# Optimization experiments

Measured on AMD Instinct MI355X. Metric: run time of the kernel, lower is better.

The kernel has to match this reference:

```python
import jax, jax.numpy as jnp
import numpy as np

K_NBR = 128        # PyG radius(max_num_neighbors=128)
NEG_FILL = -1e9    # mask value for max-aggregation over invalid neighbors


def fps(pos, m):
    # Farthest point sampling on pos [N,2] -> [m] int32 indices (start at 0).
    n = pos.shape[0]
    def step(carry, _):
        min_d2, last = carry
        d2 = jnp.sum((pos - pos[last]) ** 2, axis=-1)
        min_d2 = jnp.minimum(min_d2, d2)
        nxt = jnp.argmax(min_d2).astype(jnp.int32)
        return (min_d2, nxt), nxt
    init = (jnp.full((n,), 1e10, pos.dtype), jnp.int32(0))
    _, idxs = jax.lax.scan(step, init, None, length=m - 1)
    return jnp.concatenate([jnp.zeros((1,), jnp.int32), idxs])


def set_abstraction(x, pos, ratio, r, W, b):
    # x [B,N,C], pos [B,N,2]. FPS centers, radius neighbors (<=K), PointNetConv
    # message = Linear(cat[x_j, pos_j - pos_i]) (PyG MLP with one layer and
    # plain_last=True is a bare Linear), then max-aggregate per center.
    B, N, C = x.shape
    m = int(N * ratio)
    idx = jax.vmap(lambda p: fps(p, m))(pos)                         # [B,m]
    ctr = jnp.take_along_axis(pos, idx[..., None], axis=1)           # [B,m,2]
    d2 = jnp.sum((ctr[:, :, None, :] - pos[:, None, :, :]) ** 2, -1)  # [B,m,N]
    k = min(K_NBR, N)
    neg_d2, nbr = jax.lax.top_k(-d2, k)                              # [B,m,k]
    valid = (-neg_d2) <= r * r                                       # in-radius mask
    gather = jax.vmap(lambda a, i: a[i])                             # per-sample fancy index
    x_j = gather(x, nbr)                                             # [B,m,k,C]
    rel = gather(pos, nbr) - ctr[:, :, None, :]                      # [B,m,k,2]
    msg = jnp.concatenate([x_j, rel], axis=-1) @ W + b               # [B,m,k,F]
    msg = jnp.where(valid[..., None], msg, NEG_FILL)
    return jnp.max(msg, axis=2), ctr                                 # [B,m,F], [B,m,2]


def encoder(x, zones_ids, lf_W1, lf_b1, lf_W2, lf_b2, c1_W, c1_b, c2_W, c2_b, c3_W, c3_b):
    lf = jnp.tanh(jnp.tanh(x @ lf_W1 + lf_b1) @ lf_W2 + lf_b2)       # [B,N,64]
    h = jnp.concatenate([lf, zones_ids], axis=-1)                    # [B,N,65]
    h, pos = set_abstraction(h, x, 0.5, 0.5, c1_W, c1_b)             # [B,N/2,64]
    h, pos = set_abstraction(h, pos, 0.25, 1.0, c2_W, c2_b)          # [B,N/8,128]
    g = jnp.concatenate([h, pos], axis=-1) @ c3_W + c3_b             # [B,N/8,1024]
    gf = jnp.max(g, axis=1, keepdims=True)                           # global max pool -> [B,1,1024]
    return lf, gf


def setup_inputs():
    key = jax.random.key(0)
    ks = jax.random.split(key, 12)
    B, N = 4, 4096
    def lin(kw, kb, fi, fo):
        return (jax.random.normal(kw, (fi, fo), jnp.float32) / np.sqrt(fi),
                jax.random.normal(kb, (fo,), jnp.float32) * 0.01)
    x = jax.random.normal(ks[0], (B, N, 2), jnp.float32) * 4.0  # spread so ball(r) holds <128 pts
    zones_ids = jax.random.uniform(ks[1], (B, N, 1), jnp.float32)
    lf_W1, lf_b1 = lin(ks[2], ks[3], 2, 64)
    lf_W2, lf_b2 = lin(ks[4], ks[5], 64, 64)
    c1_W, c1_b = lin(ks[6], ks[7], 67, 64)
    c2_W, c2_b = lin(ks[8], ks[9], 66, 128)
    c3_W, c3_b = lin(ks[10], ks[11], 130, 1024)
    return {"x": x, "zones_ids": zones_ids, "lf_W1": lf_W1, "lf_b1": lf_b1,
            "lf_W2": lf_W2, "lf_b2": lf_b2, "c1_W": c1_W, "c1_b": c1_b,
            "c2_W": c2_W, "c2_b": c2_b, "c3_W": c3_W, "c3_b": c3_b}


def reference(x, zones_ids, lf_W1, lf_b1, lf_W2, lf_b2, c1_W, c1_b, c2_W, c2_b, c3_W, c3_b):
    return encoder(x, zones_ids, lf_W1, lf_b1, lf_W2, lf_b2,
                   c1_W, c1_b, c2_W, c2_b, c3_W, c3_b)
```

## Files before the change

kernel.cpp:

```cpp
#include <hip/hip_runtime.h>


constexpr int BB = 4;
constexpr int NN = 4096;
constexpr int M1 = 2048;
constexpr int M2 = 512;

__device__ __forceinline__ float d2_exact(float dx, float dy) {
    return __fadd_rn(__fmul_rn(dx, dx), __fmul_rn(dy, dy));
}

template<int CTRL>
__device__ __forceinline__ unsigned long long dpp64z(unsigned long long v) {
    unsigned lo = (unsigned)__builtin_amdgcn_update_dpp(0, (int)(unsigned)v, CTRL, 0xF, 0xF, true);
    unsigned hi = (unsigned)__builtin_amdgcn_update_dpp(0, (int)(unsigned)(v >> 32), CTRL, 0xF, 0xF, true);
    return ((unsigned long long)hi << 32) | (unsigned long long)lo;
}
template<int CTRL>
__device__ __forceinline__ void pairc(unsigned long long& t1, unsigned long long& t2) {
    unsigned long long o1 = dpp64z<CTRL>(t1);
    unsigned long long o2 = dpp64z<CTRL>(t2);
    bool g = o1 > t1;
    unsigned long long m1 = g ? o1 : t1;
    unsigned long long sm = g ? t1 : o1;
    unsigned long long cn = g ? o2 : t2;
    t2 = cn > sm ? cn : sm;
    t1 = m1;
}
__device__ __forceinline__ unsigned long long readlane64(unsigned long long v, int l) {
    unsigned lo = (unsigned)__builtin_amdgcn_readlane((int)(unsigned)v, l);
    unsigned hi = (unsigned)__builtin_amdgcn_readlane((int)(unsigned)(v >> 32), l);
    return ((unsigned long long)hi << 32) | (unsigned long long)lo;
}

__global__ __launch_bounds__(256) void k_lf_y1(
    const float2* __restrict__ x, const float* __restrict__ zones,
    const float* __restrict__ W1, const float* __restrict__ b1,
    const float* __restrict__ W2, const float* __restrict__ b2,
    const float* __restrict__ c1W, const float* __restrict__ c1b,
    float* __restrict__ out_lf, float* __restrict__ y1)
{
    __shared__ float sh[4][64];
    __shared__ float sl[4][64];
    int tid = threadIdx.x;
    int p = tid >> 6, f = tid & 63;
    size_t pt = (size_t)blockIdx.x * 4 + p;
    float2 xv = x[pt];
    float hid = tanhf(xv.x * W1[f] + xv.y * W1[64 + f] + b1[f]);
    sh[p][f] = hid;
    __syncthreads();
    float acc = b2[f];
#pragma unroll
    for (int c = 0; c < 64; ++c) acc += sh[p][c] * W2[c * 64 + f];
    float lf = tanhf(acc);
    sl[p][f] = lf;
    out_lf[pt * 64 + f] = lf;
    __syncthreads();
    float acc2 = c1b[f] + zones[pt] * c1W[64 * 64 + f]
               + xv.x * c1W[65 * 64 + f] + xv.y * c1W[66 * 64 + f];
#pragma unroll
    for (int c = 0; c < 64; ++c) acc2 += sl[p][c] * c1W[c * 64 + f];
    y1[pt * 64 + f] = acc2;
}

template<int NP, int M>
__global__ __launch_bounds__(512) void k_fps(const float2* __restrict__ pos,
                                             float* __restrict__ ctr)
{
#pragma clang fp contract(off)
    constexpr int PPT = NP / 512;
    __shared__ float2 PTS[NP];
    __shared__ float2 cent[M];
    __shared__ unsigned long long sl[2][16];
    int tid = threadIdx.x, lane = tid & 63, wv = tid >> 6;
    const float2* p = pos + (size_t)blockIdx.x * NP;

    float px[PPT], py[PPT], md[PPT];
    unsigned lowk[PPT];
#pragma unroll
    for (int s = 0; s < PPT; ++s) {
        float2 v = p[tid + s * 512];
        px[s] = v.x; py[s] = v.y; md[s] = 1e10f;
        lowk[s] = 0xFFFFFFFFu - (unsigned)(tid + s * 512);
        PTS[tid + s * 512] = v;
    }
    float2 c0 = p[0];
    if (tid == 0) cent[0] = c0;
    __syncthreads();

    float c1x = c0.x, c1y = c0.y, c2x = 0.0f, c2y = 0.0f;
    bool two = false;
    int it = 1;
    unsigned rc = 0;
    while (it < M) {
        int par = (int)(rc & 1u); ++rc;
#pragma unroll
        for (int s = 0; s < PPT; ++s)
            md[s] = fminf(md[s], d2_exact(px[s] - c1x, py[s] - c1y));
        if (two) {
#pragma unroll
            for (int s = 0; s < PPT; ++s)
                md[s] = fminf(md[s], d2_exact(px[s] - c2x, py[s] - c2y));
        }
        unsigned long long t1 = 0ull, t2 = 0ull;
#pragma unroll
        for (int s = 0; s < PPT; ++s) {
            unsigned long long key =
                ((unsigned long long)__float_as_uint(md[s]) << 32) | (unsigned long long)lowk[s];
            bool g = key > t1;
            unsigned long long ns = g ? t1 : (key > t2 ? key : t2);
            t1 = g ? key : t1;
            t2 = ns;
        }
        pairc<0x111>(t1, t2); pairc<0x112>(t1, t2); pairc<0x114>(t1, t2);
        pairc<0x118>(t1, t2); pairc<0x142>(t1, t2); pairc<0x143>(t1, t2);
        if (lane == 63) { sl[par][2 * wv] = t1; sl[par][2 * wv + 1] = t2; }
        __syncthreads();
        unsigned long long a1 = sl[par][2 * (lane & 7)];
        unsigned long long a2 = sl[par][2 * (lane & 7) + 1];
        if (lane >= 8) { a1 = 0ull; a2 = 0ull; }
        pairc<0x111>(a1, a2); pairc<0x112>(a1, a2); pairc<0x114>(a1, a2);
        unsigned long long w1 = readlane64(a1, 7);
        unsigned long long r1 = readlane64(a2, 7);
        int jw = (int)(0xFFFFFFFFu - (unsigned)w1);
        int jr = (int)(0xFFFFFFFFu - (unsigned)r1);
        float mdr = __uint_as_float((unsigned)(r1 >> 32));
        float2 wpt = PTS[jw];
        float2 rpt = PTS[jr];
        float ddx = rpt.x - wpt.x, ddy = rpt.y - wpt.y;
        float dd = (ddx * ddx) + (ddy * ddy);
        bool dbl = (it + 1 < M) && (dd >= mdr);
        if (tid == 0) { cent[it] = wpt; if (dbl) cent[it + 1] = rpt; }
        c1x = wpt.x; c1y = wpt.y; c2x = rpt.x; c2y = rpt.y;
        two = dbl;
        it += dbl ? 2 : 1;
    }
    __syncthreads();
    float2* co = (float2*)(ctr + (size_t)blockIdx.x * M * 2);
    for (int i = tid; i < M; i += 512) co[i] = cent[i];
}

__global__ __launch_bounds__(256) void k_sa(
    const float2* __restrict__ candpos, const float* __restrict__ y,
    const float* __restrict__ ctr, const float* __restrict__ W,
    int NP, int F, int relrow, float r2, float* __restrict__ hout)
{
    __shared__ int cnt;
    __shared__ int list[4096];
    int tid = threadIdx.x;
    int b = blockIdx.y;
    size_t crow = (size_t)b * gridDim.x + blockIdx.x;
    if (tid == 0) cnt = 0;
    __syncthreads();
    float cx = ctr[crow * 2], cy = ctr[crow * 2 + 1];
    const float2* cp = candpos + (size_t)b * NP;
    for (int j = tid; j < NP; j += 256) {
        float2 pj = cp[j];
        float d2 = d2_exact(pj.x - cx, pj.y - cy);
        if (d2 <= r2) { int t = atomicAdd(&cnt, 1); list[t] = j; }
    }
    __syncthreads();
    int n = cnt;
    for (int f = tid; f < F; f += 256) {
        float m = -3.0e38f;
        for (int t = 0; t < n; ++t)
            m = fmaxf(m, y[((size_t)b * NP + list[t]) * F + f]);
        float ct = cx * W[(size_t)relrow * F + f] + cy * W[(size_t)(relrow + 1) * F + f];
        hout[crow * F + f] = m - ct;
    }
}

__global__ __launch_bounds__(128) void k_y2(
    const float* __restrict__ h1, const float* __restrict__ p1,
    const float* __restrict__ W, const float* __restrict__ bb,
    float* __restrict__ y2)
{
    __shared__ float sh[64];
    size_t row = blockIdx.x;
    int f = threadIdx.x;
    if (f < 64) sh[f] = h1[row * 64 + f];
    __syncthreads();
    float acc = bb[f] + p1[row * 2] * W[64 * 128 + f]
              + p1[row * 2 + 1] * W[65 * 128 + f];
#pragma unroll
    for (int c = 0; c < 64; ++c) acc += sh[c] * W[c * 128 + f];
    y2[row * 128 + f] = acc;
}

__global__ __launch_bounds__(256) void k_g(
    const float* __restrict__ h2, const float* __restrict__ p2,
    const float* __restrict__ W3, const float* __restrict__ b3,
    float* __restrict__ part)
{
    int f = blockIdx.x * 256 + threadIdx.x;
    int b = blockIdx.z;
    int i0 = blockIdx.y * 8;
    float acc[8];
    float bbv = b3[f];
#pragma unroll
    for (int ii = 0; ii < 8; ++ii) acc[ii] = bbv;
    const float* hrow = h2 + ((size_t)b * M2 + i0) * 128;
    for (int c = 0; c < 128; ++c) {
        float w = W3[(size_t)c * 1024 + f];
#pragma unroll
        for (int ii = 0; ii < 8; ++ii) acc[ii] += hrow[ii * 128 + c] * w;
    }
    float wx = W3[(size_t)128 * 1024 + f];
    float wy = W3[(size_t)129 * 1024 + f];
    const float* prow = p2 + ((size_t)b * M2 + i0) * 2;
    float m = -3.0e38f;
#pragma unroll
    for (int ii = 0; ii < 8; ++ii) {
        float g = acc[ii] + prow[ii * 2] * wx + prow[ii * 2 + 1] * wy;
        m = fmaxf(m, g);
    }
    part[((size_t)b * 64 + blockIdx.y) * 1024 + f] = m;
}

__global__ __launch_bounds__(256) void k_gmax(const float* __restrict__ part,
                                              float* __restrict__ outg)
{
    int f = blockIdx.x * 256 + threadIdx.x;
    int b = f >> 10, fl = f & 1023;
    float m = -3.0e38f;
#pragma unroll 8
    for (int ig = 0; ig < 64; ++ig)
        m = fmaxf(m, part[((size_t)b * 64 + ig) * 1024 + fl]);
    outg[f] = m;
}

extern "C" void kernel_launch(void* const* d_in, const int* in_sizes, int n_in,
                              void* d_out, int out_size, void* d_ws, size_t ws_size,
                              hipStream_t stream)
{
    const float* x    = (const float*)d_in[0];
    const float* zon  = (const float*)d_in[1];
    const float* lfW1 = (const float*)d_in[2];
    const float* lfb1 = (const float*)d_in[3];
    const float* lfW2 = (const float*)d_in[4];
    const float* lfb2 = (const float*)d_in[5];
    const float* c1W  = (const float*)d_in[6];
    const float* c1b  = (const float*)d_in[7];
    const float* c2W  = (const float*)d_in[8];
    const float* c2b  = (const float*)d_in[9];
    const float* c3W  = (const float*)d_in[10];
    const float* c3b  = (const float*)d_in[11];
    float* out = (float*)d_out;

    char* w = (char*)d_ws;
    float* big = (float*)w;                    w += (size_t)BB * NN * 64 * 4;
    float* p1  = (float*)w;                    w += (size_t)BB * M1 * 2 * 4;
    float* h1  = (float*)w;                    w += (size_t)BB * M1 * 64 * 4;
    float* p2  = (float*)w;                    w += (size_t)BB * M2 * 2 * 4;
    float* h2  = (float*)w;                    w += (size_t)BB * M2 * 128 * 4;
    float* y1 = big, * y2 = big, * part = big;

    k_lf_y1<<<BB * NN / 4, 256, 0, stream>>>((const float2*)x, zon, lfW1, lfb1,
                                             lfW2, lfb2, c1W, c1b, out, y1);
    k_fps<NN, M1><<<BB, 512, 0, stream>>>((const float2*)x, p1);
    k_sa<<<dim3(M1, BB), 256, 0, stream>>>((const float2*)x, y1, p1, c1W,
                                           NN, 64, 65, 0.25f, h1);
    k_fps<M1, M2><<<BB, 512, 0, stream>>>((const float2*)p1, p2);
    k_y2<<<BB * M1, 128, 0, stream>>>(h1, p1, c2W, c2b, y2);
    k_sa<<<dim3(M2, BB), 256, 0, stream>>>((const float2*)p1, y2, p2, c2W,
                                           M1, 128, 64, 1.0f, h2);
    k_g<<<dim3(4, 64, BB), 256, 0, stream>>>(h2, p2, c3W, c3b, part);
    k_gmax<<<16, 256, 0, stream>>>(part, out + (size_t)BB * NN * 64);
}
```

Baseline: 1.712 ms.

## Fuse both FPS stages into one kernel and use packed float2 distance math

Merges the two farthest-point-sampling launches into a single kernel per batch. The first-stage centers stay in LDS and feed the second stage directly, which removes a launch and a global reload of the first-stage centers. The per-iteration distance and min updates now use two-wide float vectors so the compiler can emit packed FP32 instructions. The index keys are recomputed each iteration instead of held in registers, which trades a few ALU ops for lower register pressure under the new launch bounds.

After: 1.684 ms. About the same (-1.6%).

```diff
diff --git a/kernel.cpp b/kernel.cpp
--- a/kernel.cpp
+++ b/kernel.cpp
@@ -5,6 +5,8 @@
 constexpr int NN = 4096;
 constexpr int M1 = 2048;
 constexpr int M2 = 512;
+
+typedef float v2f __attribute__((ext_vector_type(2)));
 
 __device__ __forceinline__ float d2_exact(float dx, float dy) {
     return __fadd_rn(__fmul_rn(dx, dx), __fmul_rn(dy, dy));
@@ -63,30 +65,25 @@
     y1[pt * 64 + f] = acc2;
 }
 
-template<int NP, int M>
-__global__ __launch_bounds__(512) void k_fps(const float2* __restrict__ pos,
-                                             float* __restrict__ ctr)
+template<int M, int PPT>
+__device__ __forceinline__ void fps_core(
+    const float2* __restrict__ src, const float2* __restrict__ PTSl,
+    float2* __restrict__ centl, unsigned long long (&sl)[2][16],
+    int tid, int lane, int wv)
 {
 #pragma clang fp contract(off)
-    constexpr int PPT = NP / 512;
-    __shared__ float2 PTS[NP];
-    __shared__ float2 cent[M];
-    __shared__ unsigned long long sl[2][16];
-    int tid = threadIdx.x, lane = tid & 63, wv = tid >> 6;
-    const float2* p = pos + (size_t)blockIdx.x * NP;
-
-    float px[PPT], py[PPT], md[PPT];
-    unsigned lowk[PPT];
-#pragma unroll
-    for (int s = 0; s < PPT; ++s) {
-        float2 v = p[tid + s * 512];
-        px[s] = v.x; py[s] = v.y; md[s] = 1e10f;
-        lowk[s] = 0xFFFFFFFFu - (unsigned)(tid + s * 512);
-        PTS[tid + s * 512] = v;
-    }
-    float2 c0 = p[0];
-    if (tid == 0) cent[0] = c0;
-    __syncthreads();
+    constexpr int PP2 = PPT / 2;
+    v2f px2[PP2], py2[PP2], md2[PP2];
+#pragma unroll
+    for (int k = 0; k < PP2; ++k) {
+        float2 a = src[tid + (2 * k) * 512];
+        float2 b = src[tid + (2 * k + 1) * 512];
+        px2[k] = (v2f){a.x, b.x};
+        py2[k] = (v2f){a.y, b.y};
+        md2[k] = (v2f){1e10f, 1e10f};
+    }
+    float2 c0 = src[0];
+    if (tid == 0) centl[0] = c0;
 
     float c1x = c0.x, c1y = c0.y, c2x = 0.0f, c2y = 0.0f;
     bool two = false;
@@ -94,19 +91,29 @@
     unsigned rc = 0;
     while (it < M) {
         int par = (int)(rc & 1u); ++rc;
-#pragma unroll
-        for (int s = 0; s < PPT; ++s)
-            md[s] = fminf(md[s], d2_exact(px[s] - c1x, py[s] - c1y));
+        v2f vcx = (v2f){c1x, c1x}, vcy = (v2f){c1y, c1y};
+#pragma unroll
+        for (int k = 0; k < PP2; ++k) {
+            v2f dx = px2[k] - vcx, dy = py2[k] - vcy;
+            v2f d2 = (dx * dx) + (dy * dy);
+            md2[k] = __builtin_elementwise_min(md2[k], d2);
+        }
         if (two) {
-#pragma unroll
-            for (int s = 0; s < PPT; ++s)
-                md[s] = fminf(md[s], d2_exact(px[s] - c2x, py[s] - c2y));
+            v2f wcx = (v2f){c2x, c2x}, wcy = (v2f){c2y, c2y};
+#pragma unroll
+            for (int k = 0; k < PP2; ++k) {
+                v2f dx = px2[k] - wcx, dy = py2[k] - wcy;
+                v2f d2 = (dx * dx) + (dy * dy);
+                md2[k] = __builtin_elementwise_min(md2[k], d2);
+            }
         }
         unsigned long long t1 = 0ull, t2 = 0ull;
 #pragma unroll
         for (int s = 0; s < PPT; ++s) {
+            float mq = (s & 1) ? md2[s >> 1].y : md2[s >> 1].x;
             unsigned long long key =
-                ((unsigned long long)__float_as_uint(md[s]) << 32) | (unsigned long long)lowk[s];
+                ((unsigned long long)__float_as_uint(mq) << 32)
+                | (unsigned long long)(0xFFFFFFFFu - (unsigned)(tid + s * 512));
             bool g = key > t1;
             unsigned long long ns = g ? t1 : (key > t2 ? key : t2);
             t1 = g ? key : t1;
@@ -125,19 +132,41 @@
         int jw = (int)(0xFFFFFFFFu - (unsigned)w1);
         int jr = (int)(0xFFFFFFFFu - (unsigned)r1);
         float mdr = __uint_as_float((unsigned)(r1 >> 32));
-        float2 wpt = PTS[jw];
-        float2 rpt = PTS[jr];
+        float2 wpt = PTSl[jw];
+        float2 rpt = PTSl[jr];
         float ddx = rpt.x - wpt.x, ddy = rpt.y - wpt.y;
         float dd = (ddx * ddx) + (ddy * ddy);
         bool dbl = (it + 1 < M) && (dd >= mdr);
-        if (tid == 0) { cent[it] = wpt; if (dbl) cent[it + 1] = rpt; }
+        if (tid == 0) { centl[it] = wpt; if (dbl) centl[it + 1] = rpt; }
         c1x = wpt.x; c1y = wpt.y; c2x = rpt.x; c2y = rpt.y;
         two = dbl;
         it += dbl ? 2 : 1;
     }
-    __syncthreads();
-    float2* co = (float2*)(ctr + (size_t)blockIdx.x * M * 2);
-    for (int i = tid; i < M; i += 512) co[i] = cent[i];
+}
+
+__global__ __launch_bounds__(512, 2) void k_fps_fused(
+    const float2* __restrict__ pos, float* __restrict__ p1out,
+    float* __restrict__ p2out)
+{
+    __shared__ float2 PTS[NN];
+    __shared__ float2 cent1[M1];
+    __shared__ float2 cent2[M2];
+    __shared__ unsigned long long sl[2][16];
+    int tid = threadIdx.x, lane = tid & 63, wv = tid >> 6;
+    const float2* p = pos + (size_t)blockIdx.x * NN;
+
+    for (int i = tid; i < NN; i += 512) PTS[i] = p[i];
+    __syncthreads();
+
+    fps_core<M1, NN / 512>(p, PTS, cent1, sl, tid, lane, wv);
+    __syncthreads();
+    float2* o1 = (float2*)(p1out + (size_t)blockIdx.x * M1 * 2);
+    for (int i = tid; i < M1; i += 512) o1[i] = cent1[i];
+
+    fps_core<M2, M1 / 512>(cent1, cent1, cent2, sl, tid, lane, wv);
+    __syncthreads();
+    float2* o2 = (float2*)(p2out + (size_t)blockIdx.x * M2 * 2);
+    for (int i = tid; i < M2; i += 512) o2[i] = cent2[i];
 }
 
 __global__ __launch_bounds__(256) void k_sa(
@@ -257,10 +286,9 @@
 
     k_lf_y1<<<BB * NN / 4, 256, 0, stream>>>((const float2*)x, zon, lfW1, lfb1,
                                              lfW2, lfb2, c1W, c1b, out, y1);
-    k_fps<NN, M1><<<BB, 512, 0, stream>>>((const float2*)x, p1);
+    k_fps_fused<<<BB, 512, 0, stream>>>((const float2*)x, p1, p2);
     k_sa<<<dim3(M1, BB), 256, 0, stream>>>((const float2*)x, y1, p1, c1W,
                                            NN, 64, 65, 0.25f, h1);
-    k_fps<M1, M2><<<BB, 512, 0, stream>>>((const float2*)p1, p2);
     k_y2<<<BB * M1, 128, 0, stream>>>(h1, p1, c2W, c2b, y2);
     k_sa<<<dim3(M2, BB), 256, 0, stream>>>((const float2*)p1, y2, p2, c2W,
                                            M1, 128, 64, 1.0f, h2);
```
